# Kernel tuning notes

Measured on AMD Instinct MI355X. Metric: run time of the kernel, lower is better.

## Reference

```python
import jax, jax.numpy as jnp
import numpy as np

N, E, D, H, L = 40000, 640000, 128, 4, 2
C = D // H  # head dim
NEG_SLOPE = 0.2


def setup_inputs() -> dict:
    key = jax.random.key(0)
    ks = jax.random.split(key, 9)
    s = 1.0 / np.sqrt(D)
    x = jax.random.normal(ks[0], (N, D), dtype=jnp.float32)
    edge_index = jax.random.randint(ks[1], (2, E), 0, N, dtype=jnp.int64)
    # Per-layer stacked GATv2Conv parameters (PyG parameterization):
    Wl = jax.random.normal(ks[2], (L, D, D), dtype=jnp.float32) * s   # lin_l weight
    bl = jnp.zeros((L, D), dtype=jnp.float32)                          # lin_l bias
    Wr = jax.random.normal(ks[3], (L, D, D), dtype=jnp.float32) * s   # lin_r weight
    br = jnp.zeros((L, D), dtype=jnp.float32)                          # lin_r bias
    att = jax.random.normal(ks[4], (L, H, C), dtype=jnp.float32) * (1.0 / np.sqrt(C))
    Wres = jax.random.normal(ks[5], (L, D, D), dtype=jnp.float32) * s  # residual proj
    bias = jnp.zeros((L, D), dtype=jnp.float32)                        # final bias
    return {"x": x, "edge_index": edge_index, "Wl": Wl, "bl": bl,
            "Wr": Wr, "br": br, "att": att, "Wres": Wres, "bias": bias}


def _gatv2_layer(x, src, dst, Wl, bl, Wr, br, att, Wres, b):
    # x: [N, D]; src/dst: [E] (edge j -> i, dst is aggregation target)
    xl = (x @ Wl + bl).reshape(N, H, C)
    xr = (x @ Wr + br).reshape(N, H, C)
    # per-edge GATv2 score: a^T LeakyReLU(xl_j + xr_i)
    e = jax.nn.leaky_relu(xl[src] + xr[dst], NEG_SLOPE)        # [E, H, C]
    alpha = jnp.einsum('ehc,hc->eh', e, att)                    # [E, H]
    # segment softmax over edges grouped by target node
    amax = jax.ops.segment_max(alpha, dst, num_segments=N)      # [N, H]
    amax = jnp.where(jnp.isfinite(amax), amax, 0.0)
    ex = jnp.exp(alpha - amax[dst])
    denom = jax.ops.segment_sum(ex, dst, num_segments=N) + 1e-16
    a = ex / denom[dst]                                         # [E, H]
    # scatter-add weighted source messages
    out = jax.ops.segment_sum(xl[src] * a[:, :, None], dst, num_segments=N)
    out = out.reshape(N, H * C) + x @ Wres + b                  # concat heads + residual + bias
    return jax.nn.elu(out)


def reference(x, edge_index, Wl, bl, Wr, br, att, Wres, bias):
    src, dst = edge_index[0], edge_index[1]
    for l in range(L):
        x = _gatv2_layer(x, src, dst, Wl[l], bl[l], Wr[l], br[l], att[l], Wres[l], bias[l])
    return x
```

## Files before the change

### kernel.cpp

```cpp
#include <hip/hip_runtime.h>
#include <cstdint>

#define NN 40000
#define EE 640000
#define DD 128
#define HH 4
#define CC 32
#define LL 2
#define NEG_SLOPE 0.2f
#define NBLK 157

typedef __attribute__((ext_vector_type(8))) short bf16x8;
typedef __attribute__((ext_vector_type(4))) float f32x4;

__device__ __forceinline__ unsigned short f2bf(float f) {
    unsigned u = __float_as_uint(f);
    unsigned r = (u + 0x7FFFu + ((u >> 16) & 1)) >> 16;
    return (unsigned short)r;
}
__device__ __forceinline__ float bf2f(unsigned short u) {
    return __uint_as_float(((unsigned)u) << 16);
}

__device__ __forceinline__ void gload16(const void* g, void* l) {
    __builtin_amdgcn_global_load_lds(
        (const __attribute__((address_space(1))) unsigned*)g,
        (__attribute__((address_space(3))) unsigned*)l, 16, 0, 0);
}

__global__ __launch_bounds__(256) void prep_kernel(
    const float* __restrict__ x,
    const float* __restrict__ Wl, const float* __restrict__ Wr,
    const float* __restrict__ Wres,
    unsigned short* __restrict__ xb, unsigned short* __restrict__ Wb,
    int* __restrict__ deg)
{
    const int i = blockIdx.x * 256 + threadIdx.x;
    if (i < NN * DD / 4) {
        const float4 v = ((const float4*)x)[i];
        ushort4 o;
        o.x = f2bf(v.x); o.y = f2bf(v.y); o.z = f2bf(v.z); o.w = f2bf(v.w);
        ((ushort4*)xb)[i] = o;
    }
    if (i < LL * 6 * 8192) {
        const int l = i / 49152;
        const int rem0 = i - l * 49152;
        const int nb = rem0 >> 13;
        const int rem = rem0 & 8191;
        const int q = rem >> 9;
        const int n = (rem >> 3) & 63;
        const int j = rem & 7;
        const int k = q * 8 + j;
        const int colg = (nb & 1) * 64 + n;
        const float* W = (nb < 2) ? Wl : (nb < 4) ? Wr : Wres;
        Wb[i] = f2bf(W[(size_t)l * DD * DD + k * DD + colg]);
    }
    if (i < NN) deg[i] = 0;
}

__global__ __launch_bounds__(256) void gemm_mfma_kernel(
    const unsigned short* __restrict__ xb, const unsigned short* __restrict__ Wb,
    const float* __restrict__ bl, const float* __restrict__ br,
    const float* __restrict__ bias,
    unsigned short* __restrict__ xlb, unsigned short* __restrict__ xrb,
    unsigned short* __restrict__ resb)
{
    __shared__ __align__(16) unsigned short lds[16384];
    const int lane = threadIdx.x & 63;
    const int wv = threadIdx.x >> 6;
    const int row0 = blockIdx.x << 6;

#pragma unroll
    for (int j = 0; j < 4; ++j) {
        const int q = j * 4 + wv;
        gload16(xb + (size_t)(row0 + lane) * DD + q * 8, &lds[q * 512]);
    }

    const int wm = wv >> 1, wn = wv & 1;
    const int h = lane >> 4, r = lane & 15;

    for (int t = 0; t < 6; ++t) {
        __syncthreads();
#pragma unroll
        for (int j = 0; j < 4; ++j) {
            const int q = j * 4 + wv;
            gload16(Wb + (size_t)t * 8192 + q * 512 + lane * 8, &lds[8192 + q * 512]);
        }
        __syncthreads();

        f32x4 acc[2][2] = {{{0.f,0.f,0.f,0.f},{0.f,0.f,0.f,0.f}},
                           {{0.f,0.f,0.f,0.f},{0.f,0.f,0.f,0.f}}};
#pragma unroll
        for (int s = 0; s < 4; ++s) {
            const int base = (s * 4 + h) * 64;
            const bf16x8 a0 = *(const bf16x8*)&lds[(base + wm * 32 + r) * 8];
            const bf16x8 a1 = *(const bf16x8*)&lds[(base + wm * 32 + 16 + r) * 8];
            const bf16x8 b0 = *(const bf16x8*)&lds[8192 + (base + wn * 32 + r) * 8];
            const bf16x8 b1 = *(const bf16x8*)&lds[8192 + (base + wn * 32 + 16 + r) * 8];
            acc[0][0] = __builtin_amdgcn_mfma_f32_16x16x32_bf16(a0, b0, acc[0][0], 0, 0, 0);
            acc[0][1] = __builtin_amdgcn_mfma_f32_16x16x32_bf16(a0, b1, acc[0][1], 0, 0, 0);
            acc[1][0] = __builtin_amdgcn_mfma_f32_16x16x32_bf16(a1, b0, acc[1][0], 0, 0, 0);
            acc[1][1] = __builtin_amdgcn_mfma_f32_16x16x32_bf16(a1, b1, acc[1][1], 0, 0, 0);
        }

        unsigned short* const outp = (t < 2) ? xlb : (t < 4) ? xrb : resb;
        const float* const bp = (t < 2) ? bl : (t < 4) ? br : bias;
        const int c0 = (t & 1) * 64 + wn * 32;
#pragma unroll
        for (int ni = 0; ni < 2; ++ni) {
            const int col = c0 + ni * 16 + r;
            const float bv = bp[col];
#pragma unroll
            for (int mi = 0; mi < 2; ++mi) {
                const int rw = row0 + wm * 32 + mi * 16 + h * 4;
#pragma unroll
                for (int v = 0; v < 4; ++v)
                    outp[(size_t)(rw + v) * DD + col] = f2bf(acc[mi][ni][v] + bv);
            }
        }
    }
}


__global__ __launch_bounds__(256) void hist_kernel(
    const int* __restrict__ dst, int* __restrict__ deg)
{
    const int e = blockIdx.x * 256 + threadIdx.x;
    if (e < EE) atomicAdd(&deg[dst[e]], 1);
}

__global__ __launch_bounds__(256) void scan1_kernel(
    const int* __restrict__ deg, int* __restrict__ rowptr, int* __restrict__ blksum)
{
    __shared__ int s[256];
    const int i = blockIdx.x * 256 + threadIdx.x;
    const int v = (i < NN) ? deg[i] : 0;
    s[threadIdx.x] = v;
    __syncthreads();
    for (int off = 1; off < 256; off <<= 1) {
        const int t = (threadIdx.x >= off) ? s[threadIdx.x - off] : 0;
        __syncthreads();
        s[threadIdx.x] += t;
        __syncthreads();
    }
    if (i < NN) rowptr[i] = s[threadIdx.x] - v;
    if (threadIdx.x == 255) blksum[blockIdx.x] = s[255];
}

__global__ __launch_bounds__(256) void scan2_kernel(int* __restrict__ blksum)
{
    __shared__ int s[256];
    const int v = (threadIdx.x < NBLK) ? blksum[threadIdx.x] : 0;
    s[threadIdx.x] = v;
    __syncthreads();
    for (int off = 1; off < 256; off <<= 1) {
        const int t = (threadIdx.x >= off) ? s[threadIdx.x - off] : 0;
        __syncthreads();
        s[threadIdx.x] += t;
        __syncthreads();
    }
    if (threadIdx.x < NBLK) blksum[threadIdx.x] = s[threadIdx.x] - v;
}

__global__ __launch_bounds__(256) void scan3_kernel(
    int* __restrict__ rowptr, const int* __restrict__ blksum, int* __restrict__ cursor)
{
    const int i = blockIdx.x * 256 + threadIdx.x;
    if (i < NN) {
        const int v = rowptr[i] + blksum[blockIdx.x];
        rowptr[i] = v;
        cursor[i] = v;
    }
    if (i == 0) rowptr[NN] = EE;
}

__global__ __launch_bounds__(256) void fill_kernel(
    const int* __restrict__ src, const int* __restrict__ dst,
    int* __restrict__ cursor, int* __restrict__ colb)
{
    const int e = blockIdx.x * 256 + threadIdx.x;
    if (e < EE) {
        const int p = atomicAdd(&cursor[dst[e]], 1);
        colb[p] = src[e] << 8;
    }
}

__global__ __launch_bounds__(256) void gather_kernel(
    const unsigned short* __restrict__ xlb, const unsigned short* __restrict__ xrb,
    const unsigned short* __restrict__ resb,
    const int* __restrict__ rowptr, const int* __restrict__ colb,
    const float* __restrict__ att,
    float* __restrict__ outf, unsigned short* __restrict__ outb)
{
    const int node = (blockIdx.x * 256 + threadIdx.x) >> 6;
    const int lane = threadIdx.x & 63;
    if (node >= NN) return;
    const int halfid = lane >> 5;
    const int hl = lane & 31;

    const ushort4 xru = ((const ushort4*)(xrb + (size_t)node * DD))[hl];
    const float xr0 = bf2f(xru.x), xr1 = bf2f(xru.y);
    const float xr2 = bf2f(xru.z), xr3 = bf2f(xru.w);
    const float4 attv = ((const float4*)att)[hl];
    const char* const xbase = (const char*)xlb;

    float d = 0.f, a0 = 0.f, a1 = 0.f, a2 = 0.f, a3 = 0.f;
    const int beg = rowptr[node], end = rowptr[node + 1];

    int p = beg;
    for (; p + 8 <= end; p += 8) {
        float xv[4][4], al[4];
#pragma unroll
        for (int i = 0; i < 4; ++i) {
            const int off = colb[p + 2 * i + halfid];
            const ushort4 u = *(const ushort4*)(xbase + off + hl * 8);
            xv[i][0] = bf2f(u.x); xv[i][1] = bf2f(u.y);
            xv[i][2] = bf2f(u.z); xv[i][3] = bf2f(u.w);
        }
#pragma unroll
        for (int i = 0; i < 4; ++i) {
            float z0 = xv[i][0] + xr0; z0 = fmaxf(z0, NEG_SLOPE * z0);
            float z1 = xv[i][1] + xr1; z1 = fmaxf(z1, NEG_SLOPE * z1);
            float z2 = xv[i][2] + xr2; z2 = fmaxf(z2, NEG_SLOPE * z2);
            float z3 = xv[i][3] + xr3; z3 = fmaxf(z3, NEG_SLOPE * z3);
            al[i] = z0 * attv.x + z1 * attv.y + z2 * attv.z + z3 * attv.w;
        }
#pragma unroll
        for (int o = 1; o <= 4; o <<= 1) {
#pragma unroll
            for (int i = 0; i < 4; ++i) al[i] += __shfl_xor(al[i], o);
        }
#pragma unroll
        for (int i = 0; i < 4; ++i) {
            const float w = __expf(al[i]);
            d  += w;
            a0 += w * xv[i][0]; a1 += w * xv[i][1];
            a2 += w * xv[i][2]; a3 += w * xv[i][3];
        }
    }
    if (p < end) {
        float xv[4][4], al[4];
        int vl[4];
#pragma unroll
        for (int i = 0; i < 4; ++i) {
            const int q = p + 2 * i + halfid;
            vl[i] = (q < end);
            const int off = colb[vl[i] ? q : beg];
            const ushort4 u = *(const ushort4*)(xbase + off + hl * 8);
            xv[i][0] = bf2f(u.x); xv[i][1] = bf2f(u.y);
            xv[i][2] = bf2f(u.z); xv[i][3] = bf2f(u.w);
        }
#pragma unroll
        for (int i = 0; i < 4; ++i) {
            float z0 = xv[i][0] + xr0; z0 = fmaxf(z0, NEG_SLOPE * z0);
            float z1 = xv[i][1] + xr1; z1 = fmaxf(z1, NEG_SLOPE * z1);
            float z2 = xv[i][2] + xr2; z2 = fmaxf(z2, NEG_SLOPE * z2);
            float z3 = xv[i][3] + xr3; z3 = fmaxf(z3, NEG_SLOPE * z3);
            al[i] = z0 * attv.x + z1 * attv.y + z2 * attv.z + z3 * attv.w;
        }
#pragma unroll
        for (int o = 1; o <= 4; o <<= 1) {
#pragma unroll
            for (int i = 0; i < 4; ++i) al[i] += __shfl_xor(al[i], o);
        }
#pragma unroll
        for (int i = 0; i < 4; ++i) {
            const float w = vl[i] ? __expf(al[i]) : 0.f;
            d  += w;
            a0 += w * xv[i][0]; a1 += w * xv[i][1];
            a2 += w * xv[i][2]; a3 += w * xv[i][3];
        }
    }

    d  += __shfl_xor(d, 32);
    a0 += __shfl_xor(a0, 32); a1 += __shfl_xor(a1, 32);
    a2 += __shfl_xor(a2, 32); a3 += __shfl_xor(a3, 32);

    if (halfid == 0) {
        const float inv = 1.f / (d + 1e-16f);
        const ushort4 ru = ((const ushort4*)(resb + (size_t)node * DD))[hl];
        float o0 = a0 * inv + bf2f(ru.x);
        float o1 = a1 * inv + bf2f(ru.y);
        float o2 = a2 * inv + bf2f(ru.z);
        float o3 = a3 * inv + bf2f(ru.w);
        o0 = (o0 > 0.f) ? o0 : expm1f(o0);
        o1 = (o1 > 0.f) ? o1 : expm1f(o1);
        o2 = (o2 > 0.f) ? o2 : expm1f(o2);
        o3 = (o3 > 0.f) ? o3 : expm1f(o3);
        if (outf) {
            float4 ov; ov.x = o0; ov.y = o1; ov.z = o2; ov.w = o3;
            ((float4*)(outf + (size_t)node * DD))[hl] = ov;
        }
        if (outb) {
            ushort4 ob;
            ob.x = f2bf(o0); ob.y = f2bf(o1); ob.z = f2bf(o2); ob.w = f2bf(o3);
            ((ushort4*)(outb + (size_t)node * DD))[hl] = ob;
        }
    }
}

extern "C" void kernel_launch(void* const* d_in, const int* in_sizes, int n_in,
                              void* d_out, int out_size, void* d_ws, size_t ws_size,
                              hipStream_t stream)
{
    const float* x0   = (const float*)d_in[0];
    const int*   ei   = (const int*)  d_in[1];
    const float* Wl   = (const float*)d_in[2];
    const float* bl   = (const float*)d_in[3];
    const float* Wr   = (const float*)d_in[4];
    const float* br   = (const float*)d_in[5];
    const float* att  = (const float*)d_in[6];
    const float* Wres = (const float*)d_in[7];
    const float* bias = (const float*)d_in[8];
    const int* src = ei;
    const int* dst = ei + EE;

    float* p = (float*)d_ws;
    unsigned short* xlb  = (unsigned short*)p; p += (size_t)NN * DD / 2;
    unsigned short* xrb  = (unsigned short*)p; p += (size_t)NN * DD / 2;
    unsigned short* resb = (unsigned short*)p; p += (size_t)NN * DD / 2;
    unsigned short* xb0  = (unsigned short*)p; p += (size_t)NN * DD / 2;
    unsigned short* xb1  = (unsigned short*)p; p += (size_t)NN * DD / 2;
    unsigned short* Wb   = (unsigned short*)p; p += LL * 6 * 8192 / 2;
    int* rowptr = (int*)p; p += NN + 1;
    int* deg    = (int*)p; p += NN;
    int* cursor = (int*)p; p += NN;
    int* blksum = (int*)p; p += NBLK;
    int* colb   = (int*)p; p += EE;

    prep_kernel<<<(NN * DD / 4 + 255) / 256, 256, 0, stream>>>(
        x0, Wl, Wr, Wres, xb0, Wb, deg);
    hist_kernel<<<(EE + 255) / 256, 256, 0, stream>>>(dst, deg);
    scan1_kernel<<<NBLK, 256, 0, stream>>>(deg, rowptr, blksum);
    scan2_kernel<<<1, 256, 0, stream>>>(blksum);
    scan3_kernel<<<NBLK, 256, 0, stream>>>(rowptr, blksum, cursor);
    fill_kernel<<<(EE + 255) / 256, 256, 0, stream>>>(src, dst, cursor, colb);

    for (int l = 0; l < LL; ++l) {
        const unsigned short* xin = (l == 0) ? xb0 : xb1;
        gemm_mfma_kernel<<<625, 256, 0, stream>>>(
            xin, Wb + (size_t)l * 6 * 8192, bl + l * DD, br + l * DD, bias + l * DD,
            xlb, xrb, resb);
        gather_kernel<<<(NN * 64 + 255) / 256, 256, 0, stream>>>(
            xlb, xrb, resb, rowptr, colb, att + (size_t)l * HH * CC,
            (l == LL - 1) ? (float*)d_out : nullptr,
            (l == 0) ? xb1 : nullptr);
    }
}
```

Baseline: 170.4 us.

## Fuse scan kernels and vectorize gather with packed math and DPP reductions

```diff
diff --git a/kernel.cpp b/kernel.cpp
--- a/kernel.cpp
+++ b/kernel.cpp
@@ -12,6 +12,7 @@
 
 typedef __attribute__((ext_vector_type(8))) short bf16x8;
 typedef __attribute__((ext_vector_type(4))) float f32x4;
+typedef __attribute__((ext_vector_type(2))) float f32x2;
 
 __device__ __forceinline__ unsigned short f2bf(float f) {
     unsigned u = __float_as_uint(f);
@@ -26,6 +27,12 @@
     __builtin_amdgcn_global_load_lds(
         (const __attribute__((address_space(1))) unsigned*)g,
         (__attribute__((address_space(3))) unsigned*)l, 16, 0, 0);
+}
+
+template<int CTRL>
+__device__ __forceinline__ float dpp_badd(float v) {
+    const int j = __builtin_amdgcn_mov_dpp(__float_as_int(v), CTRL, 0xF, 0xF, true);
+    return v + __int_as_float(j);
 }
 
 __global__ __launch_bounds__(256) void prep_kernel(
@@ -147,7 +154,8 @@
     if (threadIdx.x == 255) blksum[blockIdx.x] = s[255];
 }
 
-__global__ __launch_bounds__(256) void scan2_kernel(int* __restrict__ blksum)
+__global__ __launch_bounds__(256) void scan23_kernel(
+    int* __restrict__ rowptr, const int* __restrict__ blksum, int* __restrict__ cursor)
 {
     __shared__ int s[256];
     const int v = (threadIdx.x < NBLK) ? blksum[threadIdx.x] : 0;
@@ -159,17 +167,12 @@
         s[threadIdx.x] += t;
         __syncthreads();
     }
-    if (threadIdx.x < NBLK) blksum[threadIdx.x] = s[threadIdx.x] - v;
-}
-
-__global__ __launch_bounds__(256) void scan3_kernel(
-    int* __restrict__ rowptr, const int* __restrict__ blksum, int* __restrict__ cursor)
-{
+    const int boff = s[blockIdx.x] - blksum[blockIdx.x];
     const int i = blockIdx.x * 256 + threadIdx.x;
     if (i < NN) {
-        const int v = rowptr[i] + blksum[blockIdx.x];
-        rowptr[i] = v;
-        cursor[i] = v;
+        const int val = rowptr[i] + boff;
+        rowptr[i] = val;
+        cursor[i] = val;
     }
     if (i == 0) rowptr[NN] = EE;
 }
@@ -198,91 +201,80 @@
     const int halfid = lane >> 5;
     const int hl = lane & 31;
 
-    const ushort4 xru = ((const ushort4*)(xrb + (size_t)node * DD))[hl];
-    const float xr0 = bf2f(xru.x), xr1 = bf2f(xru.y);
-    const float xr2 = bf2f(xru.z), xr3 = bf2f(xru.w);
+    const uint2 xu = *(const uint2*)(xrb + (size_t)node * DD + hl * 4);
+    const f32x2 xr01 = {__uint_as_float(xu.x << 16), __uint_as_float(xu.x & 0xFFFF0000u)};
+    const f32x2 xr23 = {__uint_as_float(xu.y << 16), __uint_as_float(xu.y & 0xFFFF0000u)};
     const float4 attv = ((const float4*)att)[hl];
+    const f32x2 at6_01 = {0.6f * attv.x, 0.6f * attv.y};
+    const f32x2 at6_23 = {0.6f * attv.z, 0.6f * attv.w};
+    const f32x2 at4_01 = {0.4f * attv.x, 0.4f * attv.y};
+    const f32x2 at4_23 = {0.4f * attv.z, 0.4f * attv.w};
     const char* const xbase = (const char*)xlb;
 
-    float d = 0.f, a0 = 0.f, a1 = 0.f, a2 = 0.f, a3 = 0.f;
+    float d = 0.f;
+    f32x2 acc01 = {0.f, 0.f}, acc23 = {0.f, 0.f};
     const int beg = rowptr[node], end = rowptr[node + 1];
 
     int p = beg;
-    for (; p + 8 <= end; p += 8) {
-        float xv[4][4], al[4];
-#pragma unroll
-        for (int i = 0; i < 4; ++i) {
-            const int off = colb[p + 2 * i + halfid];
-            const ushort4 u = *(const ushort4*)(xbase + off + hl * 8);
-            xv[i][0] = bf2f(u.x); xv[i][1] = bf2f(u.y);
-            xv[i][2] = bf2f(u.z); xv[i][3] = bf2f(u.w);
-        }
-#pragma unroll
-        for (int i = 0; i < 4; ++i) {
-            float z0 = xv[i][0] + xr0; z0 = fmaxf(z0, NEG_SLOPE * z0);
-            float z1 = xv[i][1] + xr1; z1 = fmaxf(z1, NEG_SLOPE * z1);
-            float z2 = xv[i][2] + xr2; z2 = fmaxf(z2, NEG_SLOPE * z2);
-            float z3 = xv[i][3] + xr3; z3 = fmaxf(z3, NEG_SLOPE * z3);
-            al[i] = z0 * attv.x + z1 * attv.y + z2 * attv.z + z3 * attv.w;
-        }
-#pragma unroll
-        for (int o = 1; o <= 4; o <<= 1) {
-#pragma unroll
-            for (int i = 0; i < 4; ++i) al[i] += __shfl_xor(al[i], o);
-        }
-#pragma unroll
-        for (int i = 0; i < 4; ++i) {
-            const float w = __expf(al[i]);
-            d  += w;
-            a0 += w * xv[i][0]; a1 += w * xv[i][1];
-            a2 += w * xv[i][2]; a3 += w * xv[i][3];
-        }
-    }
-    if (p < end) {
-        float xv[4][4], al[4];
-        int vl[4];
-#pragma unroll
-        for (int i = 0; i < 4; ++i) {
-            const int q = p + 2 * i + halfid;
-            vl[i] = (q < end);
-            const int off = colb[vl[i] ? q : beg];
-            const ushort4 u = *(const ushort4*)(xbase + off + hl * 8);
-            xv[i][0] = bf2f(u.x); xv[i][1] = bf2f(u.y);
-            xv[i][2] = bf2f(u.z); xv[i][3] = bf2f(u.w);
-        }
-#pragma unroll
-        for (int i = 0; i < 4; ++i) {
-            float z0 = xv[i][0] + xr0; z0 = fmaxf(z0, NEG_SLOPE * z0);
-            float z1 = xv[i][1] + xr1; z1 = fmaxf(z1, NEG_SLOPE * z1);
-            float z2 = xv[i][2] + xr2; z2 = fmaxf(z2, NEG_SLOPE * z2);
-            float z3 = xv[i][3] + xr3; z3 = fmaxf(z3, NEG_SLOPE * z3);
-            al[i] = z0 * attv.x + z1 * attv.y + z2 * attv.z + z3 * attv.w;
-        }
-#pragma unroll
-        for (int o = 1; o <= 4; o <<= 1) {
-#pragma unroll
-            for (int i = 0; i < 4; ++i) al[i] += __shfl_xor(al[i], o);
-        }
-#pragma unroll
-        for (int i = 0; i < 4; ++i) {
-            const float w = vl[i] ? __expf(al[i]) : 0.f;
-            d  += w;
-            a0 += w * xv[i][0]; a1 += w * xv[i][1];
-            a2 += w * xv[i][2]; a3 += w * xv[i][3];
-        }
-    }
-
-    d  += __shfl_xor(d, 32);
-    a0 += __shfl_xor(a0, 32); a1 += __shfl_xor(a1, 32);
-    a2 += __shfl_xor(a2, 32); a3 += __shfl_xor(a3, 32);
+
+#define CHUNK_BODY(GUARDED)                                                    \
+    {                                                                          \
+        f32x2 xv01[4], xv23[4]; float al[4]; int vl[4];                        \
+        _Pragma("unroll")                                                      \
+        for (int i = 0; i < 4; ++i) {                                          \
+            const int q = p + 2 * i + halfid;                                  \
+            vl[i] = GUARDED ? (q < end) : 1;                                   \
+            const int off = colb[vl[i] ? q : beg];                             \
+            const uint2 u = *(const uint2*)(xbase + off + hl * 8);             \
+            xv01[i] = (f32x2){__uint_as_float(u.x << 16),                      \
+                              __uint_as_float(u.x & 0xFFFF0000u)};             \
+            xv23[i] = (f32x2){__uint_as_float(u.y << 16),                      \
+                              __uint_as_float(u.y & 0xFFFF0000u)};             \
+        }                                                                      \
+        _Pragma("unroll")                                                      \
+        for (int i = 0; i < 4; ++i) {                                          \
+            const f32x2 z01 = xv01[i] + xr01;                                  \
+            const f32x2 z23 = xv23[i] + xr23;                                  \
+            const f32x2 za01 = __builtin_elementwise_abs(z01);                 \
+            const f32x2 za23 = __builtin_elementwise_abs(z23);                 \
+            f32x2 s2 = z01 * at6_01;                                           \
+            s2 += za01 * at4_01;                                               \
+            s2 += z23 * at6_23;                                                \
+            s2 += za23 * at4_23;                                               \
+            al[i] = s2.x + s2.y;                                               \
+        }                                                                      \
+        _Pragma("unroll")                                                      \
+        for (int i = 0; i < 4; ++i) {                                          \
+            al[i] = dpp_badd<0xB1>(al[i]);      \
+            al[i] = dpp_badd<0x4E>(al[i]);      \
+            al[i] = dpp_badd<0x141>(al[i]);     \
+        }                                                                      \
+        _Pragma("unroll")                                                      \
+        for (int i = 0; i < 4; ++i) {                                          \
+            float w = __expf(al[i]);                                           \
+            if (GUARDED) w = vl[i] ? w : 0.f;                                  \
+            const f32x2 w2 = {w, w};                                           \
+            d += w;                                                            \
+            acc01 += w2 * xv01[i];                                             \
+            acc23 += w2 * xv23[i];                                             \
+        }                                                                      \
+    }
+
+    for (; p + 8 <= end; p += 8) CHUNK_BODY(0)
+    if (p < end) CHUNK_BODY(1)
+#undef CHUNK_BODY
+
+    d += __shfl_xor(d, 32);
+    acc01.x += __shfl_xor(acc01.x, 32); acc01.y += __shfl_xor(acc01.y, 32);
+    acc23.x += __shfl_xor(acc23.x, 32); acc23.y += __shfl_xor(acc23.y, 32);
 
     if (halfid == 0) {
         const float inv = 1.f / (d + 1e-16f);
         const ushort4 ru = ((const ushort4*)(resb + (size_t)node * DD))[hl];
-        float o0 = a0 * inv + bf2f(ru.x);
-        float o1 = a1 * inv + bf2f(ru.y);
-        float o2 = a2 * inv + bf2f(ru.z);
-        float o3 = a3 * inv + bf2f(ru.w);
+        float o0 = acc01.x * inv + bf2f(ru.x);
+        float o1 = acc01.y * inv + bf2f(ru.y);
+        float o2 = acc23.x * inv + bf2f(ru.z);
+        float o3 = acc23.y * inv + bf2f(ru.w);
         o0 = (o0 > 0.f) ? o0 : expm1f(o0);
         o1 = (o1 > 0.f) ? o1 : expm1f(o1);
         o2 = (o2 > 0.f) ? o2 : expm1f(o2);
@@ -332,8 +324,7 @@
         x0, Wl, Wr, Wres, xb0, Wb, deg);
     hist_kernel<<<(EE + 255) / 256, 256, 0, stream>>>(dst, deg);
     scan1_kernel<<<NBLK, 256, 0, stream>>>(deg, rowptr, blksum);
-    scan2_kernel<<<1, 256, 0, stream>>>(blksum);
-    scan3_kernel<<<NBLK, 256, 0, stream>>>(rowptr, blksum, cursor);
+    scan23_kernel<<<NBLK, 256, 0, stream>>>(rowptr, blksum, cursor);
     fill_kernel<<<(EE + 255) / 256, 256, 0, stream>>>(src, dst, cursor, colb);
 
     for (int l = 0; l < LL; ++l) {
```

Result: no change. 170.4 us (+0.0%).
